# Kernel tuning notes

Measured on AMD Instinct MI355X. Metric: run time of the kernel, lower is better.

Reference implementation:

```python
import math
import jax, jax.numpy as jnp
import numpy as np

SIZE = 5
MUL = 16                      # multiplicity of 0e and 1o in irreps_in and irreps_out
DIM = 4 * MUL                 # 16x0e (16) + 16x1o (48) = 64
INV_SQRT3 = 1.0 / math.sqrt(3.0)          # nonzero entries of wigner_3j for (1,1,0),(0,1,1),(1,0,1)
ALPHA_0 = math.sqrt(1.0 / (2 * MUL))      # out 0e: ir.dim=1 / (two uvw paths, 16*1 elements each)
ALPHA_1 = math.sqrt(3.0 / (2 * MUL))      # out 1o: ir.dim=3 / (two uvw paths, 16*1 elements each)


def _lattice():
    # torch.linspace(-1,1,size), meshgrid 'ij'; steps=(1,1,1) keeps the full cube
    r = np.linspace(-1.0, 1.0, SIZE, dtype=np.float32)
    gx, gy, gz = np.meshgrid(r, r, r, indexing='ij')
    lat = np.stack([gx, gy, gz], axis=-1)                      # (S,S,S,3), order (x,y,z)
    d = np.linalg.norm(lat, axis=-1)
    unit = np.where(d[..., None] > 0, lat / np.maximum(d[..., None], 1e-12), 0.0)
    # e3nn spherical harmonics, normalize=True, 'component' norm; l=1 basis order (y,z,x)
    sh0 = np.ones_like(d)                                      # l=0 component-normalized
    sh1 = math.sqrt(3.0) * unit[..., [1, 2, 0]]                # (S,S,S,3)
    return jnp.asarray(d), jnp.asarray(sh0), jnp.asarray(sh1)


def soft_one_hot_linspace(x, start, end, number):
    sigma = (end - start) / (number - 1)
    values = jnp.linspace(start, end, number, dtype=x.dtype)
    return jnp.exp(-(((x[..., None] - values) / sigma) ** 2)) / 1.12


def setup_inputs() -> dict:
    key = jax.random.key(0)
    k1, k2, k3, k4 = jax.random.split(key, 4)
    return {
        'x': jax.random.normal(k1, (2, DIM, 64, 64, 64), dtype=jnp.float32),
        'lin_w0': jax.random.normal(k2, (MUL, MUL), dtype=jnp.float32),
        'lin_w1': jax.random.normal(k3, (MUL, MUL), dtype=jnp.float32),
        'tp_weight': jax.random.normal(k4, (SIZE, 4 * MUL * MUL), dtype=jnp.float32),
    }


def reference(x, lin_w0, lin_w1, tp_weight):
    d, sh0, sh1 = _lattice()
    B, _, X, Y, Z = x.shape

    # ---- self connection: e3nn Linear per irrep, scaled by 1/sqrt(fan_in) ----
    inv = 1.0 / math.sqrt(MUL)
    x0 = x[:, :MUL]                                            # (B,16,X,Y,Z) scalars
    x1 = x[:, MUL:].reshape(B, MUL, 3, X, Y, Z)                # (B,16,3,X,Y,Z) vectors
    sc0 = jnp.einsum('uw,buxyz->bwxyz', lin_w0, x0) * inv
    sc1 = jnp.einsum('uw,buixyz->bwixyz', lin_w1, x1) * inv
    sc = jnp.concatenate([sc0, sc1.reshape(B, 3 * MUL, X, Y, Z)], axis=1)

    # ---- radial weights: soft one-hot embedding @ learned weights ----
    emb = soft_one_hot_linspace(d, 0.0, 1.0, SIZE) @ tp_weight                 # (S,S,S,1024)
    emb = emb * (jnp.cos(math.pi * d) / SIZE ** 1.5)[..., None]
    mm = MUL * MUL
    wA = emb[..., 0 * mm:1 * mm].reshape(SIZE, SIZE, SIZE, MUL, MUL)  # 0e(x)0e->0e
    wB = emb[..., 1 * mm:2 * mm].reshape(SIZE, SIZE, SIZE, MUL, MUL)  # 0e(x)1o->1o
    wC = emb[..., 2 * mm:3 * mm].reshape(SIZE, SIZE, SIZE, MUL, MUL)  # 1o(x)0e->1o
    wD = emb[..., 3 * mm:4 * mm].reshape(SIZE, SIZE, SIZE, MUL, MUL)  # 1o(x)1o->0e

    # ---- tp.right(sh, weight): kernel (S,S,S, in_dim, out_dim) ----
    eye3 = jnp.eye(3, dtype=x.dtype)
    k00 = ALPHA_0 * wA * sh0[..., None, None]                                        # (g,16,16)
    k10 = (ALPHA_0 * INV_SQRT3) * jnp.einsum('...uw,...i->...uiw', wD, sh1)          # (g,16,3,16)
    k01 = (ALPHA_1 * INV_SQRT3) * jnp.einsum('...uw,...k->...uwk', wB, sh1)          # (g,16,16,3)
    k11 = (ALPHA_1 * INV_SQRT3) * jnp.einsum('...uw,ik->...uiwk',
                                             wC * sh0[..., None, None], eye3)        # (g,16,3,16,3)
    g = (SIZE, SIZE, SIZE)
    top = jnp.concatenate([k00, k01.reshape(*g, MUL, 3 * MUL)], axis=-1)             # (g,16,64)
    bot = jnp.concatenate([k10.reshape(*g, 3 * MUL, MUL),
                           k11.reshape(*g, 3 * MUL, 3 * MUL)], axis=-1)              # (g,48,64)
    kernel = jnp.concatenate([top, bot], axis=-2)                                     # (S,S,S,64,64)

    # einsum('xyzio->oixyz') then conv3d (cross-correlation, same as torch)
    kernel_oi = jnp.transpose(kernel, (4, 3, 0, 1, 2))
    p = SIZE // 2
    conv = jax.lax.conv_general_dilated(
        x, kernel_oi, window_strides=(1, 1, 1), padding=[(p, p)] * 3,
        dimension_numbers=('NCDHW', 'OIDHW', 'NCDHW'))
    return sc + 0.1 * conv
```

## Files before the change

kernel.cpp:

```cpp
#include <hip/hip_runtime.h>
#include <hip/hip_bf16.h>
#include <math.h>

typedef __bf16 bf16x8 __attribute__((ext_vector_type(8)));
typedef float  f32x4  __attribute__((ext_vector_type(4)));

#define CI_STRIDE 262144
#define Z2  68
#define CIP 72

__global__ __launch_bounds__(256) void gen_w(const float* __restrict__ tp,
                                             const float* __restrict__ lw0,
                                             const float* __restrict__ lw1,
                                             __bf16* __restrict__ Wb) {
    const int t  = blockIdx.x;
    const int dx = t / 25, dy = (t / 5) % 5, dz = t % 5;
    const float rx = -1.f + 0.5f * (float)dx;
    const float ry = -1.f + 0.5f * (float)dy;
    const float rz = -1.f + 0.5f * (float)dz;
    const float d    = sqrtf(rx * rx + ry * ry + rz * rz);
    const float invd = (d > 0.f) ? (1.f / d) : 0.f;
    const float SQRT3 = 1.7320508075688772f;
    const float sh1_0 = SQRT3 * ry * invd;
    const float sh1_1 = SQRT3 * rz * invd;
    const float sh1_2 = SQRT3 * rx * invd;
    float basis[5];
#pragma unroll
    for (int m = 0; m < 5; ++m) {
        float u = (d - 0.25f * (float)m) * 4.0f;
        basis[m] = expf(-u * u) * (1.0f / 1.12f);
    }
    const float S  = cosf(3.14159265358979323846f * d) * (1.0f / 11.180339887498949f);
    const float fA = 0.1f * 0.17677669529663687f * S;
    const float fB = 0.1f * 0.3061862178478972f * 0.5773502691896258f * S;
    const float fC = 0.1f * 0.17677669529663687f * 0.5773502691896258f * S;
    const float fD = fB;

    for (int e = threadIdx.x; e < 4096; e += 256) {
        const int co = e >> 6, ci = e & 63;
        int   tt;
        float f;
        if (ci < 16) {
            if (co < 16) { tt = ci * 16 + co; f = fA; }
            else {
                const int c = co - 16, w = c / 3, kk = c % 3;
                tt = 256 + ci * 16 + w;
                f  = fB * ((kk == 0) ? sh1_0 : (kk == 1) ? sh1_1 : sh1_2);
            }
        } else {
            const int a = ci - 16, uu = a / 3, ii = a % 3;
            const float s1i = (ii == 0) ? sh1_0 : (ii == 1) ? sh1_1 : sh1_2;
            if (co < 16) { tt = 768 + uu * 16 + co; f = fC * s1i; }
            else {
                const int c = co - 16, w = c / 3, kk = c % 3;
                tt = 512 + uu * 16 + w;
                f  = (ii == kk) ? fD : 0.0f;
            }
        }
        float E = 0.f;
#pragma unroll
        for (int m = 0; m < 5; ++m) E += basis[m] * tp[m * 1024 + tt];
        float val = f * E;
        if (t == 62) {
            if (ci < 16 && co < 16) {
                val += 0.25f * lw0[ci * 16 + co];
            } else if (ci >= 16 && co >= 16) {
                const int a = co - 16, bq = ci - 16;
                const int wq = a / 3, iq = a % 3, uq = bq / 3, iiq = bq % 3;
                if (iq == iiq) val += 0.25f * lw1[uq * 16 + wq];
            }
        }
        Wb[(size_t)t * 4096 + e] = (__bf16)val;
    }
}

__device__ __forceinline__ void stage_rows(const float* __restrict__ x, __bf16* xs,
                                           int b, int xc, int y0, int dx, int w, int l) {
    const int xp  = xc + dx - 2;
    const bool xok = (xp >= 0) && (xp < 64);
    for (int rr = w; rr < 12; rr += 8) {
        const int yp = y0 + rr - 2;
        const bool ok = xok && (yp >= 0) && (yp < 64);
        const float* src = x + (size_t)b * 64 * CI_STRIDE + (size_t)xp * 4096 + yp * 64 + l;
        __bf16* dst = xs + ((size_t)rr * Z2 + 2 + l) * CIP;
        if (ok) {
#pragma unroll
            for (int c8 = 0; c8 < 8; ++c8) {
                bf16x8 pk;
#pragma unroll
                for (int jj = 0; jj < 8; ++jj)
                    pk[jj] = (__bf16)src[(size_t)(c8 * 8 + jj) * CI_STRIDE];
                *(bf16x8*)(dst + c8 * 8) = pk;
            }
        } else {
            bf16x8 zz;
#pragma unroll
            for (int jj = 0; jj < 8; ++jj) zz[jj] = (__bf16)0.f;
#pragma unroll
            for (int c8 = 0; c8 < 8; ++c8) *(bf16x8*)(dst + c8 * 8) = zz;
        }
    }
}

__global__ __launch_bounds__(512, 2) void conv_mfma(const float* __restrict__ x,
                                                    const __bf16* __restrict__ Wb,
                                                    float* __restrict__ out) {
    __shared__ __align__(16) __bf16 xs[12 * Z2 * CIP];
    __shared__ __align__(16) __bf16 ws[2][64 * CIP];
    const int tid = threadIdx.x;
    const int l = tid & 63, w = tid >> 6;
    const int q = l >> 4, i16 = l & 15;
    const int b  = blockIdx.x >> 9;
    const int xc = (blockIdx.x >> 3) & 63;
    const int y0 = (blockIdx.x & 7) << 3;

    f32x4 acc[4][4];
#pragma unroll
    for (int mt = 0; mt < 4; ++mt)
#pragma unroll
        for (int nt = 0; nt < 4; ++nt) acc[mt][nt] = (f32x4)(0.f);

    for (int idx = tid; idx < 12 * 4 * CIP; idx += 512) {
        const int r = idx / (4 * CIP), rem = idx % (4 * CIP);
        const int zs = rem / CIP, ci = rem % CIP;
        const int zp = (zs < 2) ? zs : (64 + zs);
        xs[((size_t)r * Z2 + zp) * CIP + ci] = (__bf16)0.f;
    }

    stage_rows(x, xs, b, xc, y0, 0, w, l);

    uint4 wreg = ((const uint4*)Wb)[tid];
    *(uint4*)((__bf16*)ws[0] + (tid >> 3) * CIP + (tid & 7) * 8) = wreg;
    __syncthreads();

    for (int t = 0; t < 125; ++t) {
        const int p = t & 1;
        if (t < 124) wreg = ((const uint4*)Wb)[(size_t)(t + 1) * 512 + tid];
        const int dy = (t / 5) % 5, dz = t % 5;
        const __bf16* xb = xs + ((size_t)(w + dy) * Z2 + dz + i16) * CIP + q * 8;
        const __bf16* wb = (const __bf16*)ws[p] + i16 * CIP + q * 8;
        bf16x8 A[4][2], B[4][2];
#pragma unroll
        for (int nt = 0; nt < 4; ++nt) {
            B[nt][0] = *(const bf16x8*)(xb + nt * 16 * CIP);
            B[nt][1] = *(const bf16x8*)(xb + nt * 16 * CIP + 32);
        }
#pragma unroll
        for (int mt = 0; mt < 4; ++mt) {
            A[mt][0] = *(const bf16x8*)(wb + mt * 16 * CIP);
            A[mt][1] = *(const bf16x8*)(wb + mt * 16 * CIP + 32);
        }
#pragma unroll
        for (int mt = 0; mt < 4; ++mt)
#pragma unroll
            for (int nt = 0; nt < 4; ++nt) {
                acc[mt][nt] = __builtin_amdgcn_mfma_f32_16x16x32_bf16(A[mt][0], B[nt][0], acc[mt][nt], 0, 0, 0);
                acc[mt][nt] = __builtin_amdgcn_mfma_f32_16x16x32_bf16(A[mt][1], B[nt][1], acc[mt][nt], 0, 0, 0);
            }
        if (t < 124)
            *(uint4*)((__bf16*)ws[1 - p] + (tid >> 3) * CIP + (tid & 7) * 8) = wreg;
        __syncthreads();
        if ((t % 25) == 24 && t < 124) {
            stage_rows(x, xs, b, xc, y0, t / 25 + 1, w, l);
            __syncthreads();
        }
    }

    const size_t obase = (size_t)b * 64 * CI_STRIDE + (size_t)xc * 4096 + (size_t)(y0 + w) * 64;
#pragma unroll
    for (int mt = 0; mt < 4; ++mt)
#pragma unroll
        for (int j = 0; j < 4; ++j) {
            const int co = mt * 16 + q * 4 + j;
            float* op = out + obase + (size_t)co * CI_STRIDE + i16;
#pragma unroll
            for (int nt = 0; nt < 4; ++nt) op[nt * 16] = acc[mt][nt][j];
        }
}

extern "C" void kernel_launch(void* const* d_in, const int* in_sizes, int n_in,
                              void* d_out, int out_size, void* d_ws, size_t ws_size,
                              hipStream_t stream) {
    (void)in_sizes; (void)n_in; (void)out_size; (void)ws_size;
    const float* x   = (const float*)d_in[0];
    const float* lw0 = (const float*)d_in[1];
    const float* lw1 = (const float*)d_in[2];
    const float* tp  = (const float*)d_in[3];
    float* out = (float*)d_out;
    __bf16* Wb = (__bf16*)d_ws;

    gen_w<<<125, 256, 0, stream>>>(tp, lw0, lw1, Wb);
    conv_mfma<<<1024, 512, 0, stream>>>(x, Wb, out);
}
```

Before: 676.9 us.

## Retile conv to 16 y-rows per block, split input channels, load weights from global

Each block now covers 16 y-rows instead of 8, and each warp computes two y-rows, giving 8 N-tiles per warp. Input channels are split into two halves of 32, so the LDS input tile holds 20 rows with a 40-element padded channel stride. Weights are re-laid out per tap and half and read straight from global/L2 into registers one step ahead, which removes the LDS weight double buffer and the per-tap barrier. In exchange, the input is staged twice per block (once per channel half), accumulator registers double, and the grid halves to 512 blocks, which may lower occupancy.

```diff
diff --git a/kernel.cpp b/kernel.cpp
--- a/kernel.cpp
+++ b/kernel.cpp
@@ -3,11 +3,13 @@
 #include <math.h>
 
 typedef __bf16 bf16x8 __attribute__((ext_vector_type(8)));
+typedef __bf16 bf16x2 __attribute__((ext_vector_type(2)));
 typedef float  f32x4  __attribute__((ext_vector_type(4)));
 
 #define CI_STRIDE 262144
-#define Z2  68
-#define CIP 72
+#define B_STRIDE  16777216
+#define Z2 68
+#define CP 40
 
 __global__ __launch_bounds__(256) void gen_w(const float* __restrict__ tp,
                                              const float* __restrict__ lw0,
@@ -70,111 +72,114 @@
                 if (iq == iiq) val += 0.25f * lw1[uq * 16 + wq];
             }
         }
-        Wb[(size_t)t * 4096 + e] = (__bf16)val;
-    }
-}
-
-__device__ __forceinline__ void stage_rows(const float* __restrict__ x, __bf16* xs,
-                                           int b, int xc, int y0, int dx, int w, int l) {
-    const int xp  = xc + dx - 2;
-    const bool xok = (xp >= 0) && (xp < 64);
-    for (int rr = w; rr < 12; rr += 8) {
-        const int yp = y0 + rr - 2;
-        const bool ok = xok && (yp >= 0) && (yp < 64);
-        const float* src = x + (size_t)b * 64 * CI_STRIDE + (size_t)xp * 4096 + yp * 64 + l;
-        __bf16* dst = xs + ((size_t)rr * Z2 + 2 + l) * CIP;
-        if (ok) {
-#pragma unroll
-            for (int c8 = 0; c8 < 8; ++c8) {
-                bf16x8 pk;
-#pragma unroll
-                for (int jj = 0; jj < 8; ++jj)
-                    pk[jj] = (__bf16)src[(size_t)(c8 * 8 + jj) * CI_STRIDE];
-                *(bf16x8*)(dst + c8 * 8) = pk;
-            }
-        } else {
-            bf16x8 zz;
-#pragma unroll
-            for (int jj = 0; jj < 8; ++jj) zz[jj] = (__bf16)0.f;
-#pragma unroll
-            for (int c8 = 0; c8 < 8; ++c8) *(bf16x8*)(dst + c8 * 8) = zz;
-        }
+        Wb[((size_t)(t * 2 + (ci >> 5)) * 64 + co) * 32 + (ci & 31)] = (__bf16)val;
     }
 }
 
 __global__ __launch_bounds__(512, 2) void conv_mfma(const float* __restrict__ x,
                                                     const __bf16* __restrict__ Wb,
                                                     float* __restrict__ out) {
-    __shared__ __align__(16) __bf16 xs[12 * Z2 * CIP];
-    __shared__ __align__(16) __bf16 ws[2][64 * CIP];
+    __shared__ __align__(16) __bf16 xs[20 * Z2 * CP];
     const int tid = threadIdx.x;
     const int l = tid & 63, w = tid >> 6;
     const int q = l >> 4, i16 = l & 15;
-    const int b  = blockIdx.x >> 9;
-    const int xc = (blockIdx.x >> 3) & 63;
-    const int y0 = (blockIdx.x & 7) << 3;
+    const int b  = blockIdx.x >> 8;
+    const int xc = (blockIdx.x >> 2) & 63;
+    const int y0 = (blockIdx.x & 3) << 4;
 
-    f32x4 acc[4][4];
+    f32x4 acc[4][8];
 #pragma unroll
     for (int mt = 0; mt < 4; ++mt)
 #pragma unroll
-        for (int nt = 0; nt < 4; ++nt) acc[mt][nt] = (f32x4)(0.f);
+        for (int nt = 0; nt < 8; ++nt) acc[mt][nt] = (f32x4)(0.f);
 
-    for (int idx = tid; idx < 12 * 4 * CIP; idx += 512) {
-        const int r = idx / (4 * CIP), rem = idx % (4 * CIP);
-        const int zs = rem / CIP, ci = rem % CIP;
+    for (int idx = tid; idx < 20 * 4 * CP; idx += 512) {
+        const int r = idx / (4 * CP), rem = idx % (4 * CP);
+        const int zs = rem / CP, ci = rem % CP;
         const int zp = (zs < 2) ? zs : (64 + zs);
-        xs[((size_t)r * Z2 + zp) * CIP + ci] = (__bf16)0.f;
+        xs[((size_t)r * Z2 + zp) * CP + ci] = (__bf16)0.f;
     }
 
-    stage_rows(x, xs, b, xc, y0, 0, w, l);
+    const float* xb = x + (size_t)b * B_STRIDE;
 
-    uint4 wreg = ((const uint4*)Wb)[tid];
-    *(uint4*)((__bf16*)ws[0] + (tid >> 3) * CIP + (tid & 7) * 8) = wreg;
-    __syncthreads();
+    bf16x8 Acur[4], Anext[4];
+#pragma unroll
+    for (int mt = 0; mt < 4; ++mt)
+        Acur[mt] = *(const bf16x8*)(Wb + ((size_t)(mt * 16 + i16)) * 32 + q * 8);
 
-    for (int t = 0; t < 125; ++t) {
-        const int p = t & 1;
-        if (t < 124) wreg = ((const uint4*)Wb)[(size_t)(t + 1) * 512 + tid];
-        const int dy = (t / 5) % 5, dz = t % 5;
-        const __bf16* xb = xs + ((size_t)(w + dy) * Z2 + dz + i16) * CIP + q * 8;
-        const __bf16* wb = (const __bf16*)ws[p] + i16 * CIP + q * 8;
-        bf16x8 A[4][2], B[4][2];
+    for (int h = 0; h < 2; ++h) {
+        for (int dx = 0; dx < 5; ++dx) {
+            __syncthreads();
+            {
+                const int xp = xc + dx - 2;
+                const bool xok = (xp >= 0) && (xp < 64);
+                for (int r = w; r < 20; r += 8) {
+                    const int yp = y0 + r - 2;
+                    const bool ok = xok && (yp >= 0) && (yp < 64);
+                    const float* src = xb + (size_t)(h * 32) * CI_STRIDE
+                                     + (size_t)xp * 4096 + yp * 64 + l;
+                    __bf16* dst = xs + ((size_t)r * Z2 + 2 + l) * CP;
+                    if (ok) {
 #pragma unroll
-        for (int nt = 0; nt < 4; ++nt) {
-            B[nt][0] = *(const bf16x8*)(xb + nt * 16 * CIP);
-            B[nt][1] = *(const bf16x8*)(xb + nt * 16 * CIP + 32);
-        }
+                        for (int ci = 0; ci < 32; ci += 2) {
+                            const float a0 = src[(size_t)ci * CI_STRIDE];
+                            const float a1 = src[(size_t)(ci + 1) * CI_STRIDE];
+                            bf16x2 pk = {(__bf16)a0, (__bf16)a1};
+                            *(bf16x2*)(dst + ci) = pk;
+                        }
+                    } else {
+                        bf16x2 zz = {(__bf16)0.f, (__bf16)0.f};
 #pragma unroll
-        for (int mt = 0; mt < 4; ++mt) {
-            A[mt][0] = *(const bf16x8*)(wb + mt * 16 * CIP);
-            A[mt][1] = *(const bf16x8*)(wb + mt * 16 * CIP + 32);
-        }
+                        for (int ci = 0; ci < 32; ci += 2) *(bf16x2*)(dst + ci) = zz;
+                    }
+                }
+            }
+            __syncthreads();
+
+            for (int dydz = 0; dydz < 25; ++dydz) {
+                const int t = dx * 25 + dydz;
+                const int s = h * 125 + t;
+                {
+                    const int sn = (s < 249) ? (s + 1) : s;
+                    const int hn = sn / 125, tn = sn % 125;
+                    const __bf16* wp = Wb + ((size_t)(tn * 2 + hn) * 64 + i16) * 32 + q * 8;
 #pragma unroll
-        for (int mt = 0; mt < 4; ++mt)
+                    for (int mt = 0; mt < 4; ++mt)
+                        Anext[mt] = *(const bf16x8*)(wp + (size_t)mt * 16 * 32);
+                }
+                const int dy = dydz / 5, dz = dydz % 5;
+                const __bf16* bbase = xs + ((size_t)(2 * w + dy) * Z2 + dz + i16) * CP + q * 8;
+                bf16x8 Bf[8];
 #pragma unroll
-            for (int nt = 0; nt < 4; ++nt) {
-                acc[mt][nt] = __builtin_amdgcn_mfma_f32_16x16x32_bf16(A[mt][0], B[nt][0], acc[mt][nt], 0, 0, 0);
-                acc[mt][nt] = __builtin_amdgcn_mfma_f32_16x16x32_bf16(A[mt][1], B[nt][1], acc[mt][nt], 0, 0, 0);
+                for (int yy = 0; yy < 2; ++yy)
+#pragma unroll
+                    for (int zt = 0; zt < 4; ++zt)
+                        Bf[yy * 4 + zt] = *(const bf16x8*)(bbase + (size_t)(yy * Z2 + zt * 16) * CP);
+#pragma unroll
+                for (int mt = 0; mt < 4; ++mt)
+#pragma unroll
+                    for (int nt = 0; nt < 8; ++nt)
+                        acc[mt][nt] = __builtin_amdgcn_mfma_f32_16x16x32_bf16(
+                            Acur[mt], Bf[nt], acc[mt][nt], 0, 0, 0);
+#pragma unroll
+                for (int mt = 0; mt < 4; ++mt) Acur[mt] = Anext[mt];
             }
-        if (t < 124)
-            *(uint4*)((__bf16*)ws[1 - p] + (tid >> 3) * CIP + (tid & 7) * 8) = wreg;
-        __syncthreads();
-        if ((t % 25) == 24 && t < 124) {
-            stage_rows(x, xs, b, xc, y0, t / 25 + 1, w, l);
-            __syncthreads();
         }
     }
 
-    const size_t obase = (size_t)b * 64 * CI_STRIDE + (size_t)xc * 4096 + (size_t)(y0 + w) * 64;
+    const size_t ob = (size_t)b * B_STRIDE + (size_t)xc * 4096;
 #pragma unroll
     for (int mt = 0; mt < 4; ++mt)
 #pragma unroll
         for (int j = 0; j < 4; ++j) {
             const int co = mt * 16 + q * 4 + j;
-            float* op = out + obase + (size_t)co * CI_STRIDE + i16;
+            float* op = out + ob + (size_t)co * CI_STRIDE;
 #pragma unroll
-            for (int nt = 0; nt < 4; ++nt) op[nt * 16] = acc[mt][nt][j];
+            for (int nt = 0; nt < 8; ++nt) {
+                const int y = y0 + 2 * w + (nt >> 2);
+                const int z = (nt & 3) * 16 + i16;
+                op[y * 64 + z] = acc[mt][nt][j];
+            }
         }
 }
 
@@ -190,5 +195,5 @@
     __bf16* Wb = (__bf16*)d_ws;
 
     gen_w<<<125, 256, 0, stream>>>(tp, lw0, lw1, Wb);
-    conv_mfma<<<1024, 512, 0, stream>>>(x, Wb, out);
+    conv_mfma<<<512, 512, 0, stream>>>(x, Wb, out);
 }
```

Result: faster. 573.5 us (-15.3%).
